# Kernel optimization log

Measured on AMD Instinct MI355X. Metric: run time of the kernel, lower is better.

## Reference

```python
import jax, jax.numpy as jnp
import numpy as np

B, F, C, H, W, D = 4, 2, 16, 48, 160, 96
EPS = 1e-7


def setup_inputs() -> dict:
    key = jax.random.key(0)
    k0, k1, k2 = jax.random.split(key, 3)
    current_feats = jax.random.normal(k0, (B, C, H, W), jnp.float32)
    lookup_feats = jax.random.normal(k1, (B, F, C, H, W), jnp.float32)
    # near-identity relative poses so warps land mostly in-frame
    relative_poses = jnp.eye(4, dtype=jnp.float32)[None, None] \
        + 0.02 * jax.random.normal(k2, (B, F, 4, 4), jnp.float32)
    fx, fy, cx, cy = 0.58 * W, 1.92 * H, 0.5 * W, 0.5 * H
    Kmat = jnp.array([[fx, 0., cx, 0.], [0., fy, cy, 0.],
                      [0., 0., 1., 0.], [0., 0., 0., 1.]], jnp.float32)
    K = jnp.broadcast_to(Kmat, (B, 4, 4))
    invK = jnp.broadcast_to(jnp.linalg.inv(Kmat), (B, 4, 4))
    depth_bins = jnp.linspace(2.0, 20.0, D).astype(jnp.float32)
    return {"current_feats": current_feats, "lookup_feats": lookup_feats,
            "relative_poses": relative_poses, "K": K, "invK": invK,
            "depth_bins": depth_bins}


def _pix_coords():
    # homogeneous pixel grid [3, H*W], matching BackprojectDepth
    xs, ys = jnp.meshgrid(jnp.arange(W, dtype=jnp.float32),
                          jnp.arange(H, dtype=jnp.float32), indexing='xy')
    return jnp.stack([xs.ravel(), ys.ravel(), jnp.ones(H * W, jnp.float32)], 0)


def _interior_mask():
    m = jnp.zeros((H, W), jnp.float32).at[2:-2, 2:-2].set(1.0)
    return m.reshape(H * W)


def _bilinear_zeros(img, x, y):
    """grid_sample(mode=bilinear, padding=zeros, align_corners=True).
    img [C,H,W]; x,y [D,HW] in pixel coords. Returns [D,HW] ... [C,D,HW]."""
    x0 = jnp.floor(x); y0 = jnp.floor(y)
    fx = (x - x0)[None]; fy = (y - y0)[None]  # [1,D,HW]
    x0i = x0.astype(jnp.int32); y0i = y0.astype(jnp.int32)
    flat = img.reshape(C, H * W)

    def tap(xi, yi):
        valid = ((xi >= 0) & (xi < W) & (yi >= 0) & (yi < H)).astype(img.dtype)
        idx = jnp.clip(yi, 0, H - 1) * W + jnp.clip(xi, 0, W - 1)
        return flat[:, idx] * valid[None]  # [C,D,HW]

    return (tap(x0i, y0i) * (1 - fx) * (1 - fy)
            + tap(x0i + 1, y0i) * fx * (1 - fy)
            + tap(x0i, y0i + 1) * (1 - fx) * fy
            + tap(x0i + 1, y0i + 1) * fx * fy)


def _per_pair(cur, lf, T, Kb, invKb, depth_bins):
    # cur [C,H,W], lf [C,H,W], T/Kb/invKb [4,4]
    pix = _pix_coords()                              # [3,HW]
    rays = invKb[:3, :3] @ pix                       # [3,HW]
    pts = depth_bins[:, None, None] * rays[None]     # [D,3,HW]
    pts4 = jnp.concatenate([pts, jnp.ones((D, 1, H * W), pts.dtype)], 1)
    P = (Kb @ T)[:3]                                 # [3,4]
    cam = jnp.einsum('ij,djn->din', P, pts4)         # [D,3,HW]
    z = cam[:, 2] + EPS
    px = cam[:, 0] / z                               # [D,HW] pixel x
    py = cam[:, 1] / z                               # [D,HW] pixel y
    # torch normalizes to [-1,1] then grid_sample(align_corners=True)
    # un-normalizes back to exactly px,py; sample directly.
    warped = _bilinear_zeros(lf, px, py)             # [C,D,HW]
    edge = ((px >= 2.0) & (px <= W - 2) & (py >= 2.0) & (py <= H - 2))
    mask = edge.astype(cur.dtype) * _interior_mask()[None]  # [D,HW]
    diffs = jnp.abs(warped - cur.reshape(C, 1, H * W)).mean(0) * mask
    return diffs.reshape(D, H, W)


def reference(current_feats, lookup_feats, relative_poses, K, invK, depth_bins):
    pair = jax.vmap(_per_pair, in_axes=(None, 0, 0, None, None, None))  # over frames
    diffs = jax.vmap(pair, in_axes=(0, 0, 0, 0, 0, None))(
        current_feats, lookup_feats, relative_poses, K, invK, depth_bins)  # [B,F,D,H,W]
    valid = (relative_poses.sum((-1, -2)) != 0).astype(diffs.dtype)  # skip zero poses
    diffs = diffs * valid[:, :, None, None, None]
    cost = diffs.sum(1)                                   # [B,D,H,W]
    counts = (diffs > 0).astype(diffs.dtype).sum(1)
    cost = cost / (counts + 1e-7)
    missing = (cost == 0).astype(cost.dtype)
    cost = cost * (1 - missing) + cost.max(1, keepdims=True) * missing
    return cost, missing
```

## Files before the change

kernel.cpp:

```cpp
#include <hip/hip_runtime.h>
#include <hip/hip_fp16.h>

#define B_ 4
#define F_ 2
#define C_ 16
#define H_ 48
#define W_ 160
#define D_ 96
#define HW_ (H_*W_)
#define PIX_ 64
#define GRP_ 8
#define BINS_ (D_/GRP_)
#define NCHUNK_ (HW_/PIX_)

__global__ __launch_bounds__(256) void prep_kernel(
    const float* __restrict__ cur, const float* __restrict__ look,
    const float* __restrict__ poses, const float* __restrict__ Kmat,
    __half* __restrict__ curH, __half* __restrict__ lookH,
    float* __restrict__ mats)
{
  int tid = threadIdx.x;
  int bid = blockIdx.x;
  if (bid == 0 && tid < B_*F_) {
    int t = tid, b = t / F_;
    const float* T  = poses + t*16;
    const float* Kb = Kmat + b*16;
    float sum = 0.f;
    #pragma unroll
    for (int i = 0; i < 16; ++i) sum += T[i];
    #pragma unroll
    for (int i = 0; i < 3; ++i) {
      #pragma unroll
      for (int j = 0; j < 4; ++j) {
        float v = 0.f;
        #pragma unroll
        for (int k = 0; k < 4; ++k) v += Kb[i*4+k] * T[k*4+j];
        mats[t*16 + i*4 + j] = v;
      }
    }
    mats[t*16 + 12] = (sum != 0.f) ? 1.f : 0.f;
  }
  int px_l = tid & 127;
  int h    = tid >> 7;
  int gp   = bid*128 + px_l;
  const float* src;
  __half* dst;
  int hw, c0 = h*8;
  if (gp < B_*HW_) {
    hw = gp % HW_;
    int s = gp / HW_;
    src = cur + (size_t)s*C_*HW_ + hw;
    dst = curH + (size_t)gp*C_ + c0;
  } else {
    int j = gp - B_*HW_;
    hw = j % HW_;
    int s = j / HW_;
    src = look + (size_t)s*C_*HW_ + hw;
    dst = lookH + (size_t)j*C_ + c0;
  }
  __half2 hh[4];
  #pragma unroll
  for (int j = 0; j < 4; ++j)
    hh[j] = __floats2half2_rn(src[(size_t)(c0+2*j)*HW_], src[(size_t)(c0+2*j+1)*HW_]);
  *reinterpret_cast<uint4*>(dst) = *reinterpret_cast<uint4*>(&hh[0]);
}

__global__ __launch_bounds__(512, 4) void fused_kernel(
    const __half* __restrict__ curH, const __half* __restrict__ lookH,
    const float* __restrict__ mats, const float* __restrict__ invK,
    const float* __restrict__ dbins,
    float* __restrict__ cost, float* __restrict__ missing)
{
  int tid = threadIdx.x;
  int pix = tid & (PIX_-1);
  int grp = tid >> 6;
  int bid = blockIdx.x;
  int chunk = bid % NCHUNK_;
  int b = bid / NCHUNK_;
  int hw = chunk*PIX_ + pix;
  int x = hw % W_, y = hw / W_;
  size_t obase = ((size_t)(b*D_ + grp*BINS_))*HW_ + hw;

  float res[BINS_];
  #pragma unroll
  for (int dd = 0; dd < BINS_; ++dd) res[dd] = 0.f;
  float lmax = 0.f;
  bool interior = (x >= 2 && x < W_-2 && y >= 2 && y < H_-2);
  if (interior) {
    const float* iK = invK + b*16;
    float xf = (float)x, yf = (float)y;
    float r0 = iK[0]*xf + iK[1]*yf + iK[2];
    float r1 = iK[4]*xf + iK[5]*yf + iK[6];
    float r2 = iK[8]*xf + iK[9]*yf + iK[10];
    __half2 cc2[8];
    {
      const uint4* cur4 = reinterpret_cast<const uint4*>(curH + (size_t)(b*HW_ + hw)*C_);
      *reinterpret_cast<uint4*>(&cc2[0]) = cur4[0];
      *reinterpret_cast<uint4*>(&cc2[4]) = cur4[1];
    }
    float Mv[2][13];
    #pragma unroll
    for (int f = 0; f < F_; ++f) {
      const float* Mt = mats + (b*F_+f)*16;
      #pragma unroll
      for (int i = 0; i < 13; ++i) Mv[f][i] = Mt[i];
    }
    #pragma unroll
    for (int dd = 0; dd < BINS_; ++dd) {
      float dep = dbins[grp*BINS_ + dd];
      float p0 = dep*r0, p1 = dep*r1, p2 = dep*r2;
      const __half* bases[F_];
      float w00f[F_], w10f[F_], w01f[F_], w11f[F_];
      bool okf[F_];
      #pragma unroll
      for (int f = 0; f < F_; ++f) {
        float camx = Mv[f][0]*p0 + Mv[f][1]*p1 + Mv[f][2] *p2 + Mv[f][3];
        float camy = Mv[f][4]*p0 + Mv[f][5]*p1 + Mv[f][6] *p2 + Mv[f][7];
        float camz = Mv[f][8]*p0 + Mv[f][9]*p1 + Mv[f][10]*p2 + Mv[f][11];
        float z  = camz + 1e-7f;
        float px = camx / z;
        float py = camy / z;
        okf[f] = (Mv[f][12] != 0.f) && (px >= 2.f) && (px <= (float)(W_-2))
                                    && (py >= 2.f) && (py <= (float)(H_-2));
        float x0 = floorf(px), y0 = floorf(py);
        float fx = px - x0, fy = py - y0;
        fx = fminf(fmaxf(fx, 0.f), 1.f);
        fy = fminf(fmaxf(fy, 0.f), 1.f);
        int xi = min(max((int)x0, 0), W_-2);
        int yi = min(max((int)y0, 0), H_-2);
        bases[f] = lookH + ((size_t)((b*F_+f)*HW_) + yi*W_ + xi)*C_;
        w00f[f] = (1.f-fx)*(1.f-fy); w10f[f] = fx*(1.f-fy);
        w01f[f] = (1.f-fx)*fy;       w11f[f] = fx*fy;
      }
      uint4 t[16];
      #pragma unroll
      for (int f = 0; f < F_; ++f) {
        const uint4* rr0 = reinterpret_cast<const uint4*>(bases[f]);
        const uint4* rr1 = reinterpret_cast<const uint4*>(bases[f] + W_*C_);
        #pragma unroll
        for (int i = 0; i < 4; ++i) t[f*8+i]   = rr0[i];
        #pragma unroll
        for (int i = 0; i < 4; ++i) t[f*8+4+i] = rr1[i];
      }
      float costsum = 0.f, cnt = 0.f;
      #pragma unroll
      for (int f = 0; f < F_; ++f) {
        __half2 w00h = __float2half2_rn(w00f[f]);
        __half2 w10h = __float2half2_rn(w10f[f]);
        __half2 w01h = __float2half2_rn(w01f[f]);
        __half2 w11h = __float2half2_rn(w11f[f]);
        const __half2* a00 = reinterpret_cast<const __half2*>(&t[f*8+0]);
        const __half2* a10 = reinterpret_cast<const __half2*>(&t[f*8+2]);
        const __half2* a01 = reinterpret_cast<const __half2*>(&t[f*8+4]);
        const __half2* a11 = reinterpret_cast<const __half2*>(&t[f*8+6]);
        __half2 acc0 = __float2half2_rn(0.f);
        __half2 acc1 = __float2half2_rn(0.f);
        #pragma unroll
        for (int i = 0; i < 8; ++i) {
          __half2 v = __hmul2(w00h, a00[i]);
          v = __hfma2(w10h, a10[i], v);
          v = __hfma2(w01h, a01[i], v);
          v = __hfma2(w11h, a11[i], v);
          __half2 dsub = __habs2(__hsub2(v, cc2[i]));
          if (i & 1) acc1 = __hadd2(acc1, dsub);
          else       acc0 = __hadd2(acc0, dsub);
        }
        float2 f0 = __half22float2(acc0);
        float2 f1 = __half22float2(acc1);
        float s = (f0.x + f0.y) + (f1.x + f1.y);
        float diffs = s * (1.f/16.f);
        diffs = okf[f] ? diffs : 0.f;
        costsum += diffs;
        cnt     += (diffs > 0.f) ? 1.f : 0.f;
      }
      float r = costsum / (cnt + 1e-7f);
      res[dd] = r;
      lmax = fmaxf(lmax, r);
    }
  }

  __shared__ float lmaxs[GRP_][PIX_];
  lmaxs[grp][pix] = lmax;
  __syncthreads();
  float pmax = lmaxs[0][pix];
  #pragma unroll
  for (int g = 1; g < GRP_; ++g) pmax = fmaxf(pmax, lmaxs[g][pix]);

  #pragma unroll
  for (int dd = 0; dd < BINS_; ++dd) {
    size_t o = obase + (size_t)dd*HW_;
    float v = res[dd];
    float miss = (v == 0.f) ? 1.f : 0.f;
    __builtin_nontemporal_store(miss ? pmax : v, &cost[o]);
    __builtin_nontemporal_store(miss, &missing[o]);
  }
}

extern "C" void kernel_launch(void* const* d_in, const int* in_sizes, int n_in,
                              void* d_out, int out_size, void* d_ws, size_t ws_size,
                              hipStream_t stream) {
  const float* cur   = (const float*)d_in[0];
  const float* look  = (const float*)d_in[1];
  const float* poses = (const float*)d_in[2];
  const float* Km    = (const float*)d_in[3];
  const float* invK  = (const float*)d_in[4];
  const float* dbins = (const float*)d_in[5];

  float* out_cost = (float*)d_out;
  float* out_miss = out_cost + (size_t)B_*D_*HW_;

  char*   ws    = (char*)d_ws;
  float*  mats  = (float*)ws;
  __half* curH  = (__half*)(ws + 1024);
  __half* lookH = (__half*)(ws + 1024 + (size_t)B_*HW_*C_*2);

  prep_kernel<<<(B_*HW_ + B_*F_*HW_)/128, 256, 0, stream>>>(
      cur, look, poses, Km, curH, lookH, mats);
  fused_kernel<<<B_*NCHUNK_, 512, 0, stream>>>(
      curH, lookH, mats, invK, dbins, out_cost, out_miss);
}
```

Before: 40.62 us.

## Store lookup features as interleaved row pairs for contiguous bilinear taps

The prep kernel now writes lookup features in a duplicated row-pair layout, with two copies offset by one row, so all four bilinear taps for a sample sit in one contiguous 128-byte span. The fused kernel loads eight consecutive uint4 values per frame instead of two separate row reads, and the tap pointers are reordered to match. This is meant to reduce the number of cache lines and memory transactions per gather. In exchange the workspace for lookup features doubles and the prep kernel writes twice as much.

```diff
diff --git a/kernel.cpp b/kernel.cpp
--- a/kernel.cpp
+++ b/kernel.cpp
@@ -12,11 +12,12 @@
 #define GRP_ 8
 #define BINS_ (D_/GRP_)
 #define NCHUNK_ (HW_/PIX_)
+#define NPAIR_ 24
 
 __global__ __launch_bounds__(256) void prep_kernel(
     const float* __restrict__ cur, const float* __restrict__ look,
     const float* __restrict__ poses, const float* __restrict__ Kmat,
-    __half* __restrict__ curH, __half* __restrict__ lookH,
+    __half* __restrict__ curH, __half* __restrict__ pairH,
     float* __restrict__ mats)
 {
   int tid = threadIdx.x;
@@ -43,30 +44,41 @@
   int px_l = tid & 127;
   int h    = tid >> 7;
   int gp   = bid*128 + px_l;
-  const float* src;
-  __half* dst;
-  int hw, c0 = h*8;
   if (gp < B_*HW_) {
-    hw = gp % HW_;
-    int s = gp / HW_;
-    src = cur + (size_t)s*C_*HW_ + hw;
-    dst = curH + (size_t)gp*C_ + c0;
+    int hw = gp % HW_, s = gp / HW_;
+    const float* src = cur + (size_t)s*C_*HW_ + hw;
+    int c0 = h*8;
+    __half2 hh[4];
+    #pragma unroll
+    for (int j = 0; j < 4; ++j)
+      hh[j] = __floats2half2_rn(src[(size_t)(c0+2*j)*HW_], src[(size_t)(c0+2*j+1)*HW_]);
+    *reinterpret_cast<uint4*>(curH + (size_t)gp*C_ + c0) = *reinterpret_cast<uint4*>(&hh[0]);
   } else {
     int j = gp - B_*HW_;
-    hw = j % HW_;
-    int s = j / HW_;
-    src = look + (size_t)s*C_*HW_ + hw;
-    dst = lookH + (size_t)j*C_ + c0;
-  }
-  __half2 hh[4];
-  #pragma unroll
-  for (int j = 0; j < 4; ++j)
-    hh[j] = __floats2half2_rn(src[(size_t)(c0+2*j)*HW_], src[(size_t)(c0+2*j+1)*HW_]);
-  *reinterpret_cast<uint4*>(dst) = *reinterpret_cast<uint4*>(&hh[0]);
+    int hw = j % HW_, s = j / HW_;
+    int x = hw % W_, y = hw / W_;
+    const float* src = look + (size_t)s*C_*HW_ + hw;
+    int c0 = h*8;
+    __half2 hh[4];
+    #pragma unroll
+    for (int jj = 0; jj < 4; ++jj)
+      hh[jj] = __floats2half2_rn(src[(size_t)(c0+2*jj)*HW_], src[(size_t)(c0+2*jj+1)*HW_]);
+    uint4 val = *reinterpret_cast<uint4*>(&hh[0]);
+    {
+      size_t off = ((((size_t)(s*2 + 0)*NPAIR_ + (y>>1))*W_ + x)*32) + (size_t)(y&1)*16 + h*8;
+      *reinterpret_cast<uint4*>(pairH + off) = val;
+    }
+    if (y >= 1) {
+      int p1   = (y & 1) ? (y>>1) : ((y>>1) - 1);
+      int slot = (y & 1) ? 0 : 1;
+      size_t off = ((((size_t)(s*2 + 1)*NPAIR_ + p1)*W_ + x)*32) + (size_t)slot*16 + h*8;
+      *reinterpret_cast<uint4*>(pairH + off) = val;
+    }
+  }
 }
 
 __global__ __launch_bounds__(512, 4) void fused_kernel(
-    const __half* __restrict__ curH, const __half* __restrict__ lookH,
+    const __half* __restrict__ curH, const __half* __restrict__ pairH,
     const float* __restrict__ mats, const float* __restrict__ invK,
     const float* __restrict__ dbins,
     float* __restrict__ cost, float* __restrict__ missing)
@@ -109,7 +121,7 @@
     for (int dd = 0; dd < BINS_; ++dd) {
       float dep = dbins[grp*BINS_ + dd];
       float p0 = dep*r0, p1 = dep*r1, p2 = dep*r2;
-      const __half* bases[F_];
+      const uint4* bases[F_];
       float w00f[F_], w10f[F_], w01f[F_], w11f[F_];
       bool okf[F_];
       #pragma unroll
@@ -128,19 +140,18 @@
         fy = fminf(fmaxf(fy, 0.f), 1.f);
         int xi = min(max((int)x0, 0), W_-2);
         int yi = min(max((int)y0, 0), H_-2);
-        bases[f] = lookH + ((size_t)((b*F_+f)*HW_) + yi*W_ + xi)*C_;
+        int c  = yi & 1;
+        int p  = yi >> 1;
+        bases[f] = reinterpret_cast<const uint4*>(pairH)
+                 + (((size_t)((b*F_+f)*2 + c)*NPAIR_ + p)*W_ + xi)*4;
         w00f[f] = (1.f-fx)*(1.f-fy); w10f[f] = fx*(1.f-fy);
         w01f[f] = (1.f-fx)*fy;       w11f[f] = fx*fy;
       }
       uint4 t[16];
       #pragma unroll
       for (int f = 0; f < F_; ++f) {
-        const uint4* rr0 = reinterpret_cast<const uint4*>(bases[f]);
-        const uint4* rr1 = reinterpret_cast<const uint4*>(bases[f] + W_*C_);
         #pragma unroll
-        for (int i = 0; i < 4; ++i) t[f*8+i]   = rr0[i];
-        #pragma unroll
-        for (int i = 0; i < 4; ++i) t[f*8+4+i] = rr1[i];
+        for (int i = 0; i < 8; ++i) t[f*8+i] = bases[f][i];
       }
       float costsum = 0.f, cnt = 0.f;
       #pragma unroll
@@ -150,8 +161,8 @@
         __half2 w01h = __float2half2_rn(w01f[f]);
         __half2 w11h = __float2half2_rn(w11f[f]);
         const __half2* a00 = reinterpret_cast<const __half2*>(&t[f*8+0]);
-        const __half2* a10 = reinterpret_cast<const __half2*>(&t[f*8+2]);
-        const __half2* a01 = reinterpret_cast<const __half2*>(&t[f*8+4]);
+        const __half2* a01 = reinterpret_cast<const __half2*>(&t[f*8+2]);
+        const __half2* a10 = reinterpret_cast<const __half2*>(&t[f*8+4]);
         const __half2* a11 = reinterpret_cast<const __half2*>(&t[f*8+6]);
         __half2 acc0 = __float2half2_rn(0.f);
         __half2 acc1 = __float2half2_rn(0.f);
@@ -212,10 +223,10 @@
   char*   ws    = (char*)d_ws;
   float*  mats  = (float*)ws;
   __half* curH  = (__half*)(ws + 1024);
-  __half* lookH = (__half*)(ws + 1024 + (size_t)B_*HW_*C_*2);
+  __half* pairH = (__half*)(ws + 1024 + (size_t)B_*HW_*C_*2);
 
   prep_kernel<<<(B_*HW_ + B_*F_*HW_)/128, 256, 0, stream>>>(
-      cur, look, poses, Km, curH, lookH, mats);
+      cur, look, poses, Km, curH, pairH, mats);
   fused_kernel<<<B_*NCHUNK_, 512, 0, stream>>>(
-      curH, lookH, mats, invK, dbins, out_cost, out_miss);
+      curH, pairH, mats, invK, dbins, out_cost, out_miss);
 }
```

Measured after the change: 57.68 us. +42.0%, slower.

## Split channels across two lanes per pixel with shuffle reduction

Applied to the files above, without the earlier changes.

Each pixel is now handled by two adjacent lanes, each gathering and blending 8 of the 16 half-precision channels, and the partial sums are combined with a cross-lane shuffle. Blocks cover 32 pixels instead of 64, which doubles the block count and halves per-thread gather loads and registers. The aim is more memory parallelism and occupancy for the bilinear gathers. The cost is that the projection math is duplicated across both lanes, a shuffle is added per frame, and half the lanes sit idle during the output stores.

```diff
diff --git a/kernel.cpp b/kernel.cpp
--- a/kernel.cpp
+++ b/kernel.cpp
@@ -8,7 +8,7 @@
 #define W_ 160
 #define D_ 96
 #define HW_ (H_*W_)
-#define PIX_ 64
+#define PIX_ 32
 #define GRP_ 8
 #define BINS_ (D_/GRP_)
 #define NCHUNK_ (HW_/PIX_)
@@ -71,13 +71,15 @@
     const float* __restrict__ dbins,
     float* __restrict__ cost, float* __restrict__ missing)
 {
-  int tid = threadIdx.x;
-  int pix = tid & (PIX_-1);
-  int grp = tid >> 6;
-  int bid = blockIdx.x;
+  int tid  = threadIdx.x;
+  int lane = tid & 63;
+  int px_l = lane >> 1;
+  int h    = lane & 1;
+  int grp  = tid >> 6;
+  int bid  = blockIdx.x;
   int chunk = bid % NCHUNK_;
   int b = bid / NCHUNK_;
-  int hw = chunk*PIX_ + pix;
+  int hw = chunk*PIX_ + px_l;
   int x = hw % W_, y = hw / W_;
   size_t obase = ((size_t)(b*D_ + grp*BINS_))*HW_ + hw;
 
@@ -92,12 +94,9 @@
     float r0 = iK[0]*xf + iK[1]*yf + iK[2];
     float r1 = iK[4]*xf + iK[5]*yf + iK[6];
     float r2 = iK[8]*xf + iK[9]*yf + iK[10];
-    __half2 cc2[8];
-    {
-      const uint4* cur4 = reinterpret_cast<const uint4*>(curH + (size_t)(b*HW_ + hw)*C_);
-      *reinterpret_cast<uint4*>(&cc2[0]) = cur4[0];
-      *reinterpret_cast<uint4*>(&cc2[4]) = cur4[1];
-    }
+    __half2 cc2[4];
+    *reinterpret_cast<uint4*>(&cc2[0]) =
+        *reinterpret_cast<const uint4*>(curH + (size_t)(b*HW_ + hw)*C_ + h*8);
     float Mv[2][13];
     #pragma unroll
     for (int f = 0; f < F_; ++f) {
@@ -128,19 +127,18 @@
         fy = fminf(fmaxf(fy, 0.f), 1.f);
         int xi = min(max((int)x0, 0), W_-2);
         int yi = min(max((int)y0, 0), H_-2);
-        bases[f] = lookH + ((size_t)((b*F_+f)*HW_) + yi*W_ + xi)*C_;
+        bases[f] = lookH + ((size_t)((b*F_+f)*HW_) + yi*W_ + xi)*C_ + h*8;
         w00f[f] = (1.f-fx)*(1.f-fy); w10f[f] = fx*(1.f-fy);
         w01f[f] = (1.f-fx)*fy;       w11f[f] = fx*fy;
       }
-      uint4 t[16];
+      uint4 t[8];
       #pragma unroll
       for (int f = 0; f < F_; ++f) {
-        const uint4* rr0 = reinterpret_cast<const uint4*>(bases[f]);
-        const uint4* rr1 = reinterpret_cast<const uint4*>(bases[f] + W_*C_);
-        #pragma unroll
-        for (int i = 0; i < 4; ++i) t[f*8+i]   = rr0[i];
-        #pragma unroll
-        for (int i = 0; i < 4; ++i) t[f*8+4+i] = rr1[i];
+        const __half* bp = bases[f];
+        t[f*4+0] = *reinterpret_cast<const uint4*>(bp);
+        t[f*4+1] = *reinterpret_cast<const uint4*>(bp + C_);
+        t[f*4+2] = *reinterpret_cast<const uint4*>(bp + W_*C_);
+        t[f*4+3] = *reinterpret_cast<const uint4*>(bp + W_*C_ + C_);
       }
       float costsum = 0.f, cnt = 0.f;
       #pragma unroll
@@ -149,14 +147,14 @@
         __half2 w10h = __float2half2_rn(w10f[f]);
         __half2 w01h = __float2half2_rn(w01f[f]);
         __half2 w11h = __float2half2_rn(w11f[f]);
-        const __half2* a00 = reinterpret_cast<const __half2*>(&t[f*8+0]);
-        const __half2* a10 = reinterpret_cast<const __half2*>(&t[f*8+2]);
-        const __half2* a01 = reinterpret_cast<const __half2*>(&t[f*8+4]);
-        const __half2* a11 = reinterpret_cast<const __half2*>(&t[f*8+6]);
+        const __half2* a00 = reinterpret_cast<const __half2*>(&t[f*4+0]);
+        const __half2* a10 = reinterpret_cast<const __half2*>(&t[f*4+1]);
+        const __half2* a01 = reinterpret_cast<const __half2*>(&t[f*4+2]);
+        const __half2* a11 = reinterpret_cast<const __half2*>(&t[f*4+3]);
         __half2 acc0 = __float2half2_rn(0.f);
         __half2 acc1 = __float2half2_rn(0.f);
         #pragma unroll
-        for (int i = 0; i < 8; ++i) {
+        for (int i = 0; i < 4; ++i) {
           __half2 v = __hmul2(w00h, a00[i]);
           v = __hfma2(w10h, a10[i], v);
           v = __hfma2(w01h, a01[i], v);
@@ -167,7 +165,8 @@
         }
         float2 f0 = __half22float2(acc0);
         float2 f1 = __half22float2(acc1);
-        float s = (f0.x + f0.y) + (f1.x + f1.y);
+        float s_half = (f0.x + f0.y) + (f1.x + f1.y);
+        float s = s_half + __shfl_xor(s_half, 1, 64);
         float diffs = s * (1.f/16.f);
         diffs = okf[f] ? diffs : 0.f;
         costsum += diffs;
@@ -180,19 +179,21 @@
   }
 
   __shared__ float lmaxs[GRP_][PIX_];
-  lmaxs[grp][pix] = lmax;
+  if (h == 0) lmaxs[grp][px_l] = lmax;
   __syncthreads();
-  float pmax = lmaxs[0][pix];
+  float pmax = lmaxs[0][px_l];
   #pragma unroll
-  for (int g = 1; g < GRP_; ++g) pmax = fmaxf(pmax, lmaxs[g][pix]);
-
-  #pragma unroll
-  for (int dd = 0; dd < BINS_; ++dd) {
-    size_t o = obase + (size_t)dd*HW_;
-    float v = res[dd];
-    float miss = (v == 0.f) ? 1.f : 0.f;
-    __builtin_nontemporal_store(miss ? pmax : v, &cost[o]);
-    __builtin_nontemporal_store(miss, &missing[o]);
+  for (int g = 1; g < GRP_; ++g) pmax = fmaxf(pmax, lmaxs[g][px_l]);
+
+  if (h == 0) {
+    #pragma unroll
+    for (int dd = 0; dd < BINS_; ++dd) {
+      size_t o = obase + (size_t)dd*HW_;
+      float v = res[dd];
+      float miss = (v == 0.f) ? 1.f : 0.f;
+      __builtin_nontemporal_store(miss ? pmax : v, &cost[o]);
+      __builtin_nontemporal_store(miss, &missing[o]);
+    }
   }
 }
 
```

Measured after the change: 56.41 us. 38.9% more time.
